# Kernel tuning notes

Measured on AMD Instinct MI355X. Metric: run time of the kernel, lower is better.

## Reference

```python
import jax, jax.numpy as jnp
import numpy as np

EMB = 1024
HEADS = 16
HEAD_DIM = EMB // HEADS


def setup_inputs() -> dict:
    key = jax.random.key(0)
    ks = jax.random.split(key, 6)
    B, T, D = 4, 2048, EMB
    s = 1.0 / np.sqrt(D)
    return {
        "x": jax.random.normal(ks[0], (B, T, D), dtype=jnp.float32),
        "Wq": jax.random.normal(ks[1], (D, D), dtype=jnp.float32) * s,
        "Wk": jax.random.normal(ks[2], (D, D), dtype=jnp.float32) * s,
        "Wv": jax.random.normal(ks[3], (D, D), dtype=jnp.float32) * s,
        "Wo": jax.random.normal(ks[4], (D, D), dtype=jnp.float32) * s,
        "bo": jax.random.normal(ks[5], (D,), dtype=jnp.float32) * 0.01,
    }


def reference(x, Wq, Wk, Wv, Wo, bo):
    B, T, D = x.shape
    H, Hd = HEADS, HEAD_DIM
    # torch Linear: x @ W.T ; here W stored [out,in]
    def heads(W):
        return (x @ W.T).reshape(B, T, H, Hd).transpose(0, 2, 1, 3)  # [B,H,T,Hd]
    Q, K, V = heads(Wq), heads(Wk), heads(Wv)
    scores = jnp.einsum("bhqd,bhkd->bhqk", Q, K) / np.sqrt(Hd)
    causal = jnp.triu(jnp.ones((T, T), dtype=bool), k=1)
    scores = jnp.where(causal, -jnp.inf, scores)
    weights = jax.nn.softmax(scores, axis=-1)  # dropout rate 0 -> identity
    ctx = jnp.einsum("bhqk,bhkd->bhqd", weights, V)
    ctx = ctx.transpose(0, 2, 1, 3).reshape(B, T, D)
    return ctx @ Wo.T + bo
```

## Files before the change

### kernel.cpp

```cpp
#include <hip/hip_runtime.h>

typedef short bf16x8 __attribute__((ext_vector_type(8)));
typedef float f32x4 __attribute__((ext_vector_type(4)));
typedef unsigned short u16;
typedef unsigned int u32;

__device__ __forceinline__ u16 f2b(float x) {
  union { float f; u32 u; } c; c.f = x;
  u32 r = (c.u + 0x7FFFu + ((c.u >> 16) & 1u)) >> 16;
  return (u16)r;
}

__device__ __forceinline__ float fexp2(float x) {
  return __builtin_amdgcn_exp2f(x);
}

__device__ __forceinline__ void glds16(const void* g, void* l) {
  __builtin_amdgcn_global_load_lds(
      (const __attribute__((address_space(1))) u32*)g,
      (__attribute__((address_space(3))) u32*)l, 16, 0, 0);
}

__global__ void cvt_all(const float* __restrict__ x, const float* __restrict__ Wq,
                        const float* __restrict__ Wk, const float* __restrict__ Wv,
                        const float* __restrict__ Wo, u16* __restrict__ xb,
                        u16* __restrict__ wqkvb, u16* __restrict__ wob, float qscale) {
  const int i = blockIdx.x * blockDim.x + threadIdx.x;
  const float* src;
  u16* dst;
  float scale = 1.0f;
  int off;
  if (i < 2097152) {
    src = x; dst = xb; off = i;
  } else {
    const int j = i - 2097152;
    const int wsel = j >> 18;
    off = j & 262143;
    if (wsel == 0)      { src = Wq; dst = wqkvb;            scale = qscale; }
    else if (wsel == 1) { src = Wk; dst = wqkvb + 1048576; }
    else if (wsel == 2) { src = Wv; dst = wqkvb + 2097152; }
    else                { src = Wo; dst = wob; }
  }
  float4 v = reinterpret_cast<const float4*>(src)[off];
  ushort4 o;
  o.x = f2b(v.x * scale); o.y = f2b(v.y * scale);
  o.z = f2b(v.z * scale); o.w = f2b(v.w * scale);
  reinterpret_cast<ushort4*>(dst)[off] = o;
}

template<int MODE>
__global__ __launch_bounds__(512, 2)
void gemm2(const u16* __restrict__ A, const u16* __restrict__ Bm,
           u16* __restrict__ Cq, u16* __restrict__ Ck, u16* __restrict__ Cvt,
           float* __restrict__ Cf, const float* __restrict__ bias) {
  constexpr int K = 1024, NKT = K / 64;
  __shared__ __attribute__((aligned(16))) u16 lds[3][24576];
  const int tid = threadIdx.x;
  const int w = tid >> 6;
  const int l = tid & 63;
  const int wm = w >> 2, wn = w & 3;
  const int lr = l & 15, lg = l >> 4;
  const int brow = blockIdx.x * 128;
  const int bcol = blockIdx.y * 256;
  const int wg = w * 64;

  const u16* Ab = A + (size_t)brow * K;
  const u16* Bb = Bm + (size_t)bcol * K;
  int gA[2], lA[2], gB[4], lB[4];
#pragma unroll
  for (int i = 0; i < 2; ++i) {
    const int q = i * 512 + tid;
    const int r = q >> 3, s = (q & 7) ^ (r & 7);
    gA[i] = r * K + s * 8;
    lA[i] = (i * 512 + wg) * 8;
  }
#pragma unroll
  for (int i = 0; i < 4; ++i) {
    const int q = i * 512 + tid;
    const int r = q >> 3, s = (q & 7) ^ (r & 7);
    gB[i] = r * K + s * 8;
    lB[i] = 8192 + (i * 512 + wg) * 8;
  }

  int aoff[4][2], boff[4][2];
#pragma unroll
  for (int m = 0; m < 4; ++m) {
    const int row = wm * 64 + m * 16 + lr;
#pragma unroll
    for (int kk = 0; kk < 2; ++kk)
      aoff[m][kk] = row * 64 + (((kk * 4 + lg) ^ (row & 7)) * 8);
  }
#pragma unroll
  for (int n = 0; n < 4; ++n) {
    const int row = wn * 64 + n * 16 + lr;
#pragma unroll
    for (int kk = 0; kk < 2; ++kk)
      boff[n][kk] = 8192 + row * 64 + (((kk * 4 + lg) ^ (row & 7)) * 8);
  }

  f32x4 acc[4][4] = {};

#pragma unroll
  for (int i = 0; i < 2; ++i) glds16(Ab + gA[i], &lds[0][lA[i]]);
#pragma unroll
  for (int i = 0; i < 4; ++i) glds16(Bb + gB[i], &lds[0][lB[i]]);
#pragma unroll
  for (int i = 0; i < 2; ++i) glds16(Ab + gA[i] + 64, &lds[1][lA[i]]);
#pragma unroll
  for (int i = 0; i < 4; ++i) glds16(Bb + gB[i] + 64, &lds[1][lB[i]]);
  asm volatile("s_waitcnt vmcnt(6)" ::: "memory");
  asm volatile("s_barrier" ::: "memory");

  int bi = 0;
  for (int kt = 0; kt < NKT; ++kt) {
    const u16* Lb = lds[bi];
    const int bs = (bi + 2 >= 3) ? (bi - 1) : (bi + 2);
    const bool st = (kt + 2 < NKT);
    const int ko = (kt + 2) * 64;

    bf16x8 a[4][2], b01[2][2];
#pragma unroll
    for (int m = 0; m < 4; ++m)
#pragma unroll
      for (int kk = 0; kk < 2; ++kk)
        a[m][kk] = *reinterpret_cast<const bf16x8*>(&Lb[aoff[m][kk]]);
#pragma unroll
    for (int n = 0; n < 2; ++n)
#pragma unroll
      for (int kk = 0; kk < 2; ++kk)
        b01[n][kk] = *reinterpret_cast<const bf16x8*>(&Lb[boff[n][kk]]);
    if (st) {
      glds16(Ab + gA[0] + ko, &lds[bs][lA[0]]);
      glds16(Ab + gA[1] + ko, &lds[bs][lA[1]]);
      glds16(Bb + gB[0] + ko, &lds[bs][lB[0]]);
    }
    asm volatile("s_barrier" ::: "memory");
    asm volatile("s_waitcnt lgkmcnt(0)" ::: "memory");
    __builtin_amdgcn_sched_barrier(0);
    __builtin_amdgcn_s_setprio(1);
#pragma unroll
    for (int m = 0; m < 4; ++m)
#pragma unroll
      for (int n = 0; n < 2; ++n)
#pragma unroll
        for (int kk = 0; kk < 2; ++kk)
          acc[m][n] = __builtin_amdgcn_mfma_f32_16x16x32_bf16(a[m][kk], b01[n][kk], acc[m][n], 0, 0, 0);
    __builtin_amdgcn_s_setprio(0);
    asm volatile("s_barrier" ::: "memory");

    bf16x8 b23[2][2];
#pragma unroll
    for (int n = 0; n < 2; ++n)
#pragma unroll
      for (int kk = 0; kk < 2; ++kk)
        b23[n][kk] = *reinterpret_cast<const bf16x8*>(&Lb[boff[n + 2][kk]]);
    if (st) {
      glds16(Bb + gB[1] + ko, &lds[bs][lB[1]]);
      glds16(Bb + gB[2] + ko, &lds[bs][lB[2]]);
      glds16(Bb + gB[3] + ko, &lds[bs][lB[3]]);
    }
    if (kt + 1 < NKT) {
      if (st) asm volatile("s_waitcnt vmcnt(6)" ::: "memory");
      else    asm volatile("s_waitcnt vmcnt(0)" ::: "memory");
    }
    asm volatile("s_barrier" ::: "memory");
    asm volatile("s_waitcnt lgkmcnt(0)" ::: "memory");
    __builtin_amdgcn_sched_barrier(0);
    __builtin_amdgcn_s_setprio(1);
#pragma unroll
    for (int m = 0; m < 4; ++m)
#pragma unroll
      for (int n = 0; n < 2; ++n)
#pragma unroll
        for (int kk = 0; kk < 2; ++kk)
          acc[m][n + 2] = __builtin_amdgcn_mfma_f32_16x16x32_bf16(a[m][kk], b23[n][kk], acc[m][n + 2], 0, 0, 0);
    __builtin_amdgcn_s_setprio(0);
    asm volatile("s_barrier" ::: "memory");

    bi = (bi + 1 >= 3) ? 0 : bi + 1;
  }

  if (MODE == 0) {
    const int seg = blockIdx.y >> 2;
    const int cbase = (blockIdx.y & 3) * 256;
    if (seg < 2) {
      u16* dst = (seg == 0) ? Cq : Ck;
#pragma unroll
      for (int m = 0; m < 4; ++m) {
        const size_t r = (size_t)(brow + wm * 64 + m * 16 + lg * 4);
#pragma unroll
        for (int n = 0; n < 4; ++n) {
          const int c = cbase + wn * 64 + n * 16 + lr;
#pragma unroll
          for (int j = 0; j < 4; ++j)
            dst[(r + j) * 1024 + c] = f2b(acc[m][n][j]);
        }
      }
    } else {
#pragma unroll
      for (int n = 0; n < 4; ++n) {
        const int c = cbase + wn * 64 + n * 16 + lr;
        const int hh = c >> 6, dd = c & 63;
#pragma unroll
        for (int m = 0; m < 4; ++m) {
          const int r0 = brow + wm * 64 + m * 16 + lg * 4;
#pragma unroll
          for (int j = 0; j < 4; ++j) {
            const int r = r0 + j;
            const int bt = r >> 11, tt = r & 2047;
            Cvt[((size_t)((bt * 16 + hh) * 64 + dd)) * 2048 + tt] = f2b(acc[m][n][j]);
          }
        }
      }
    }
  } else {
#pragma unroll
    for (int m = 0; m < 4; ++m) {
      const size_t r = (size_t)(brow + wm * 64 + m * 16 + lg * 4);
#pragma unroll
      for (int n = 0; n < 4; ++n) {
        const int c = bcol + wn * 64 + n * 16 + lr;
        const float bv = bias[c];
#pragma unroll
        for (int j = 0; j < 4; ++j)
          Cf[(r + j) * 1024 + c] = acc[m][n][j] + bv;
      }
    }
  }
}

__global__ __launch_bounds__(512, 2)
void attn_kernel(const u16* __restrict__ qb, const u16* __restrict__ kb,
                 const u16* __restrict__ vt, u16* __restrict__ ctx) {
  __shared__ __attribute__((aligned(16))) u16 Ks[2][4096];
  __shared__ __attribute__((aligned(16))) u16 Vs[2][4096];
  __shared__ __attribute__((aligned(16))) u16 Ps[8 * 2048];
  const int bid = blockIdx.x;
  const int chunk = bid >> 6;
  const int qt = (chunk < 4) ? (7 - chunk) : (chunk - 4);
  const int bh = bid & 63;
  const int bb = bh >> 4, h = bh & 15;
  const int tid = threadIdx.x, w = tid >> 6, l = tid & 63;
  const int lr = l & 15, lg = l >> 4;
  const int Qw = qt * 256 + w * 32;
  const int kvr = tid >> 3;
  const int gv = tid & 7;
  const int kvc = gv * 8;
  const int pgW = ((gv ^ (kvr & 7)) * 8);

  int prd[2];
#pragma unroll
  for (int kc = 0; kc < 2; ++kc) prd[kc] = ((kc * 4 + lg) ^ (lr & 7)) * 8;

  bf16x8 qf[2][2];
#pragma unroll
  for (int mi = 0; mi < 2; ++mi)
#pragma unroll
    for (int kc = 0; kc < 2; ++kc)
      qf[mi][kc] = *reinterpret_cast<const bf16x8*>(
          &qb[(size_t)(bb * 2048 + Qw + mi * 16 + lr) * 1024 + h * 64 + kc * 32 + lg * 8]);

  f32x4 oacc[2][4] = {};
  float lsum[2][4] = {};

  const int ntiles = 4 * qt + 4;

  bf16x8 kr, vr;
  kr = *reinterpret_cast<const bf16x8*>(&kb[(size_t)(bb * 2048 + kvr) * 1024 + h * 64 + kvc]);
  vr = *reinterpret_cast<const bf16x8*>(&vt[(size_t)(bh * 64 + kvr) * 2048 + kvc]);
  *reinterpret_cast<bf16x8*>(&Ks[0][kvr * 64 + pgW]) = kr;
  *reinterpret_cast<bf16x8*>(&Vs[0][kvr * 64 + pgW]) = vr;
  __syncthreads();
  kr = *reinterpret_cast<const bf16x8*>(&kb[(size_t)(bb * 2048 + 64 + kvr) * 1024 + h * 64 + kvc]);
  vr = *reinterpret_cast<const bf16x8*>(&vt[(size_t)(bh * 64 + kvr) * 2048 + 64 + kvc]);

  for (int t = 0; t < ntiles; ++t) {
    const int c0 = t * 64;
    const int cur = t & 1;

    if (c0 < Qw + 32) {
      const bool diag = (c0 + 63 > Qw);

      f32x4 sacc[2][4] = {};
      __builtin_amdgcn_s_setprio(1);
#pragma unroll
      for (int kc = 0; kc < 2; ++kc)
#pragma unroll
        for (int nj = 0; nj < 4; ++nj) {
          bf16x8 kf = *reinterpret_cast<const bf16x8*>(
              &Ks[cur][(nj * 16 + lr) * 64 + prd[kc]]);
#pragma unroll
          for (int mi = 0; mi < 2; ++mi)
            sacc[mi][nj] = __builtin_amdgcn_mfma_f32_16x16x32_bf16(qf[mi][kc], kf, sacc[mi][nj], 0, 0, 0);
        }
      __builtin_amdgcn_s_setprio(0);

#pragma unroll
      for (int mi = 0; mi < 2; ++mi) {
        if (diag) {
#pragma unroll
          for (int nj = 0; nj < 4; ++nj) {
            const int col = c0 + nj * 16 + lr;
#pragma unroll
            for (int j = 0; j < 4; ++j) {
              const int row = Qw + mi * 16 + lg * 4 + j;
              if (col > row) sacc[mi][nj][j] = -1e30f;
            }
          }
        }
#pragma unroll
        for (int nj = 0; nj < 4; ++nj) {
          const int cchunk = nj * 2 + (lr >> 3);
          const int coff = lr & 7;
#pragma unroll
          for (int j = 0; j < 4; ++j) {
            const float p = fexp2(sacc[mi][nj][j]);
            lsum[mi][j] += p;
            const int rowP = mi * 16 + lg * 4 + j;
            Ps[w * 2048 + rowP * 64 + ((cchunk ^ (rowP & 7)) * 8) + coff] = f2b(p);
          }
        }
      }

      __builtin_amdgcn_s_setprio(1);
#pragma unroll
      for (int kc = 0; kc < 2; ++kc) {
        bf16x8 pf[2];
#pragma unroll
        for (int mi = 0; mi < 2; ++mi) {
          const int rowP = mi * 16 + lr;
          const int cj = kc * 4 + lg;
          pf[mi] = *reinterpret_cast<const bf16x8*>(
              &Ps[w * 2048 + rowP * 64 + ((cj ^ (rowP & 7)) * 8)]);
        }
#pragma unroll
        for (int nd = 0; nd < 4; ++nd) {
          bf16x8 vf = *reinterpret_cast<const bf16x8*>(
              &Vs[cur][(nd * 16 + lr) * 64 + prd[kc]]);
#pragma unroll
          for (int mi = 0; mi < 2; ++mi)
            oacc[mi][nd] = __builtin_amdgcn_mfma_f32_16x16x32_bf16(pf[mi], vf, oacc[mi][nd], 0, 0, 0);
        }
      }
      __builtin_amdgcn_s_setprio(0);
    }

    if (t + 1 < ntiles) {
      *reinterpret_cast<bf16x8*>(&Ks[cur ^ 1][kvr * 64 + pgW]) = kr;
      *reinterpret_cast<bf16x8*>(&Vs[cur ^ 1][kvr * 64 + pgW]) = vr;
    }
    __syncthreads();
    if (t + 2 < ntiles) {
      const int c0n = c0 + 128;
      kr = *reinterpret_cast<const bf16x8*>(
          &kb[(size_t)(bb * 2048 + c0n + kvr) * 1024 + h * 64 + kvc]);
      vr = *reinterpret_cast<const bf16x8*>(
          &vt[(size_t)(bh * 64 + kvr) * 2048 + c0n + kvc]);
    }
  }

#pragma unroll
  for (int mi = 0; mi < 2; ++mi) {
#pragma unroll
    for (int x = 1; x < 16; x <<= 1)
#pragma unroll
      for (int j = 0; j < 4; ++j) lsum[mi][j] += __shfl_xor(lsum[mi][j], x, 64);
#pragma unroll
    for (int j = 0; j < 4; ++j) {
      const float inv = 1.0f / lsum[mi][j];
      const size_t r = (size_t)(bb * 2048 + Qw + mi * 16 + lg * 4 + j);
#pragma unroll
      for (int nd = 0; nd < 4; ++nd)
        ctx[r * 1024 + h * 64 + nd * 16 + lr] = f2b(oacc[mi][nd][j] * inv);
    }
  }
}

extern "C" void kernel_launch(void* const* d_in, const int* in_sizes, int n_in,
                              void* d_out, int out_size, void* d_ws, size_t ws_size,
                              hipStream_t stream) {
  const float* x = (const float*)d_in[0];
  const float* Wq = (const float*)d_in[1];
  const float* Wk = (const float*)d_in[2];
  const float* Wv = (const float*)d_in[3];
  const float* Wo = (const float*)d_in[4];
  const float* bo = (const float*)d_in[5];
  float* out = (float*)d_out;

  char* ws = (char*)d_ws;
  u16* xb = (u16*)(ws);
  u16* qb = (u16*)(ws + (16u << 20));
  u16* kb = (u16*)(ws + (32u << 20));
  u16* vtb = (u16*)(ws + (64u << 20));
  u16* wqkvb = (u16*)(ws + (80u << 20));
  u16* wob = (u16*)(ws + (88u << 20));

  const float qscale = 0.125f * 1.4426950408889634f;
  cvt_all<<<12288, 256, 0, stream>>>(x, Wq, Wk, Wv, Wo, xb, wqkvb, wob, qscale);

  gemm2<0><<<dim3(64, 12), 512, 0, stream>>>(xb, wqkvb, qb, kb, vtb, nullptr, nullptr);
  attn_kernel<<<512, 512, 0, stream>>>(qb, kb, vtb, xb);
  gemm2<1><<<dim3(64, 4), 512, 0, stream>>>(xb, wob, nullptr, nullptr, nullptr, out, bo);
}
```

Measured before the change: 172.5 us.

## Add 128x384-tile QKV GEMM and halve attention block size to 4 waves

Adds a new QKV projection kernel that uses 128x384 output tiles with K-step 32 and a double-buffered global-to-LDS load. This cuts the grid to 512 blocks (one wave on the device) instead of 768. The attention kernel moves from 512-thread blocks covering 256 query rows to 256-thread blocks covering 128 rows with occupancy 3. Blocks are scheduled heaviest-first by query tile, which should improve load balance for the causal workload. The output projection is split into its own kernel and is unchanged. Risks include the smaller K-step raising barrier overhead in the GEMM and smaller attention blocks reloading K/V tiles more often.

```diff
diff --git a/kernel.cpp b/kernel.cpp
--- a/kernel.cpp
+++ b/kernel.cpp
@@ -48,11 +48,109 @@
   reinterpret_cast<ushort4*>(dst)[off] = o;
 }
 
-template<int MODE>
 __global__ __launch_bounds__(512, 2)
-void gemm2(const u16* __restrict__ A, const u16* __restrict__ Bm,
-           u16* __restrict__ Cq, u16* __restrict__ Ck, u16* __restrict__ Cvt,
-           float* __restrict__ Cf, const float* __restrict__ bias) {
+void gemm4(const u16* __restrict__ A, const u16* __restrict__ Bm,
+           u16* __restrict__ Cq, u16* __restrict__ Ck, u16* __restrict__ Cvt) {
+  constexpr int K = 1024, NKT = 32;
+  __shared__ __attribute__((aligned(16))) u16 lds[2][16384];
+  const int tid = threadIdx.x;
+  const int w = tid >> 6, l = tid & 63;
+  const int wm = w >> 2, wn = w & 3;
+  const int lr = l & 15, lg = l >> 4;
+  const int brow = blockIdx.x * 128;
+  const int bcol = blockIdx.y * 384;
+  const u16* Ab = A + (size_t)brow * K;
+  const u16* Bb = Bm + (size_t)bcol * K;
+
+  int gA, gBo[3];
+  {
+    const int r = tid >> 2, p = tid & 3;
+    gA = r * K + ((p ^ ((r >> 1) & 3)) * 8);
+  }
+#pragma unroll
+  for (int j = 0; j < 3; ++j) {
+    const int gb = j * 512 + tid;
+    const int r = gb >> 2, p = gb & 3;
+    gBo[j] = r * K + ((p ^ ((r >> 1) & 3)) * 8);
+  }
+
+  int a_off[4], b_off[6];
+#pragma unroll
+  for (int m = 0; m < 4; ++m) {
+    const int row = wm * 64 + m * 16 + lr;
+    a_off[m] = row * 32 + ((lg ^ ((row >> 1) & 3)) * 8);
+  }
+#pragma unroll
+  for (int n = 0; n < 6; ++n) {
+    const int row = wn * 96 + n * 16 + lr;
+    b_off[n] = 4096 + row * 32 + ((lg ^ ((row >> 1) & 3)) * 8);
+  }
+
+  f32x4 acc[4][6] = {};
+
+  glds16(Ab + gA, &lds[0][w * 512]);
+#pragma unroll
+  for (int j = 0; j < 3; ++j) glds16(Bb + gBo[j], &lds[0][4096 + j * 4096 + w * 512]);
+  asm volatile("s_waitcnt vmcnt(0)" ::: "memory");
+  asm volatile("s_barrier" ::: "memory");
+
+  for (int kt = 0; kt < NKT; ++kt) {
+    const int cur = kt & 1;
+    const u16* Lb = lds[cur];
+    u16* Sb = lds[cur ^ 1];
+    if (kt + 1 < NKT) {
+      const int ko = (kt + 1) * 32;
+      glds16(Ab + gA + ko, &Sb[w * 512]);
+#pragma unroll
+      for (int j = 0; j < 3; ++j) glds16(Bb + gBo[j] + ko, &Sb[4096 + j * 4096 + w * 512]);
+    }
+    bf16x8 a[4], b[6];
+#pragma unroll
+    for (int m = 0; m < 4; ++m) a[m] = *reinterpret_cast<const bf16x8*>(&Lb[a_off[m]]);
+#pragma unroll
+    for (int n = 0; n < 6; ++n) b[n] = *reinterpret_cast<const bf16x8*>(&Lb[b_off[n]]);
+    __builtin_amdgcn_s_setprio(1);
+#pragma unroll
+    for (int m = 0; m < 4; ++m)
+#pragma unroll
+      for (int n = 0; n < 6; ++n)
+        acc[m][n] = __builtin_amdgcn_mfma_f32_16x16x32_bf16(a[m], b[n], acc[m][n], 0, 0, 0);
+    __builtin_amdgcn_s_setprio(0);
+    asm volatile("s_waitcnt vmcnt(0)" ::: "memory");
+    asm volatile("s_barrier" ::: "memory");
+  }
+
+#pragma unroll
+  for (int n = 0; n < 6; ++n) {
+    const int c = bcol + wn * 96 + n * 16 + lr;
+    const int seg = c >> 10, cs = c & 1023;
+    if (seg < 2) {
+      u16* dst = (seg == 0) ? Cq : Ck;
+#pragma unroll
+      for (int m = 0; m < 4; ++m) {
+        const int r0 = brow + wm * 64 + m * 16 + lg * 4;
+#pragma unroll
+        for (int j = 0; j < 4; ++j)
+          dst[(size_t)(r0 + j) * 1024 + cs] = f2b(acc[m][n][j]);
+      }
+    } else {
+      const int hh = cs >> 6, dd = cs & 63;
+#pragma unroll
+      for (int m = 0; m < 4; ++m) {
+        const int r0 = brow + wm * 64 + m * 16 + lg * 4;
+#pragma unroll
+        for (int j = 0; j < 4; ++j) {
+          const int r = r0 + j, bt = r >> 11, tt = r & 2047;
+          Cvt[((size_t)((bt * 16 + hh) * 64 + dd)) * 2048 + tt] = f2b(acc[m][n][j]);
+        }
+      }
+    }
+  }
+}
+
+__global__ __launch_bounds__(512, 2)
+void gemm2o(const u16* __restrict__ A, const u16* __restrict__ Bm,
+            float* __restrict__ Cf, const float* __restrict__ bias) {
   constexpr int K = 1024, NKT = K / 64;
   __shared__ __attribute__((aligned(16))) u16 lds[3][24576];
   const int tid = threadIdx.x;
@@ -180,69 +278,33 @@
     bi = (bi + 1 >= 3) ? 0 : bi + 1;
   }
 
-  if (MODE == 0) {
-    const int seg = blockIdx.y >> 2;
-    const int cbase = (blockIdx.y & 3) * 256;
-    if (seg < 2) {
-      u16* dst = (seg == 0) ? Cq : Ck;
-#pragma unroll
-      for (int m = 0; m < 4; ++m) {
-        const size_t r = (size_t)(brow + wm * 64 + m * 16 + lg * 4);
-#pragma unroll
-        for (int n = 0; n < 4; ++n) {
-          const int c = cbase + wn * 64 + n * 16 + lr;
-#pragma unroll
-          for (int j = 0; j < 4; ++j)
-            dst[(r + j) * 1024 + c] = f2b(acc[m][n][j]);
-        }
-      }
-    } else {
-#pragma unroll
-      for (int n = 0; n < 4; ++n) {
-        const int c = cbase + wn * 64 + n * 16 + lr;
-        const int hh = c >> 6, dd = c & 63;
-#pragma unroll
-        for (int m = 0; m < 4; ++m) {
-          const int r0 = brow + wm * 64 + m * 16 + lg * 4;
-#pragma unroll
-          for (int j = 0; j < 4; ++j) {
-            const int r = r0 + j;
-            const int bt = r >> 11, tt = r & 2047;
-            Cvt[((size_t)((bt * 16 + hh) * 64 + dd)) * 2048 + tt] = f2b(acc[m][n][j]);
-          }
-        }
-      }
-    }
-  } else {
-#pragma unroll
-    for (int m = 0; m < 4; ++m) {
-      const size_t r = (size_t)(brow + wm * 64 + m * 16 + lg * 4);
-#pragma unroll
-      for (int n = 0; n < 4; ++n) {
-        const int c = bcol + wn * 64 + n * 16 + lr;
-        const float bv = bias[c];
-#pragma unroll
-        for (int j = 0; j < 4; ++j)
-          Cf[(r + j) * 1024 + c] = acc[m][n][j] + bv;
-      }
-    }
-  }
-}
-
-__global__ __launch_bounds__(512, 2)
+#pragma unroll
+  for (int m = 0; m < 4; ++m) {
+    const size_t r = (size_t)(brow + wm * 64 + m * 16 + lg * 4);
+#pragma unroll
+    for (int n = 0; n < 4; ++n) {
+      const int c = bcol + wn * 64 + n * 16 + lr;
+      const float bv = bias[c];
+#pragma unroll
+      for (int j = 0; j < 4; ++j)
+        Cf[(r + j) * 1024 + c] = acc[m][n][j] + bv;
+    }
+  }
+}
+
+__global__ __launch_bounds__(256, 3)
 void attn_kernel(const u16* __restrict__ qb, const u16* __restrict__ kb,
                  const u16* __restrict__ vt, u16* __restrict__ ctx) {
   __shared__ __attribute__((aligned(16))) u16 Ks[2][4096];
   __shared__ __attribute__((aligned(16))) u16 Vs[2][4096];
-  __shared__ __attribute__((aligned(16))) u16 Ps[8 * 2048];
+  __shared__ __attribute__((aligned(16))) u16 Ps[4 * 2048];
   const int bid = blockIdx.x;
-  const int chunk = bid >> 6;
-  const int qt = (chunk < 4) ? (7 - chunk) : (chunk - 4);
+  const int qt = 15 - (bid >> 6);
   const int bh = bid & 63;
   const int bb = bh >> 4, h = bh & 15;
   const int tid = threadIdx.x, w = tid >> 6, l = tid & 63;
   const int lr = l & 15, lg = l >> 4;
-  const int Qw = qt * 256 + w * 32;
+  const int Qw = qt * 128 + w * 32;
   const int kvr = tid >> 3;
   const int gv = tid & 7;
   const int kvc = gv * 8;
@@ -263,16 +325,29 @@
   f32x4 oacc[2][4] = {};
   float lsum[2][4] = {};
 
-  const int ntiles = 4 * qt + 4;
-
-  bf16x8 kr, vr;
-  kr = *reinterpret_cast<const bf16x8*>(&kb[(size_t)(bb * 2048 + kvr) * 1024 + h * 64 + kvc]);
-  vr = *reinterpret_cast<const bf16x8*>(&vt[(size_t)(bh * 64 + kvr) * 2048 + kvc]);
-  *reinterpret_cast<bf16x8*>(&Ks[0][kvr * 64 + pgW]) = kr;
-  *reinterpret_cast<bf16x8*>(&Vs[0][kvr * 64 + pgW]) = vr;
+  const int ntiles = 2 * qt + 2;
+
+  bf16x8 kr[2], vr[2];
+#pragma unroll
+  for (int it = 0; it < 2; ++it) {
+    kr[it] = *reinterpret_cast<const bf16x8*>(
+        &kb[(size_t)(bb * 2048 + it * 32 + kvr) * 1024 + h * 64 + kvc]);
+    vr[it] = *reinterpret_cast<const bf16x8*>(
+        &vt[(size_t)(bh * 64 + it * 32 + kvr) * 2048 + kvc]);
+  }
+#pragma unroll
+  for (int it = 0; it < 2; ++it) {
+    *reinterpret_cast<bf16x8*>(&Ks[0][(it * 32 + kvr) * 64 + pgW]) = kr[it];
+    *reinterpret_cast<bf16x8*>(&Vs[0][(it * 32 + kvr) * 64 + pgW]) = vr[it];
+  }
   __syncthreads();
-  kr = *reinterpret_cast<const bf16x8*>(&kb[(size_t)(bb * 2048 + 64 + kvr) * 1024 + h * 64 + kvc]);
-  vr = *reinterpret_cast<const bf16x8*>(&vt[(size_t)(bh * 64 + kvr) * 2048 + 64 + kvc]);
+#pragma unroll
+  for (int it = 0; it < 2; ++it) {
+    kr[it] = *reinterpret_cast<const bf16x8*>(
+        &kb[(size_t)(bb * 2048 + 64 + it * 32 + kvr) * 1024 + h * 64 + kvc]);
+    vr[it] = *reinterpret_cast<const bf16x8*>(
+        &vt[(size_t)(bh * 64 + it * 32 + kvr) * 2048 + 64 + kvc]);
+  }
 
   for (int t = 0; t < ntiles; ++t) {
     const int c0 = t * 64;
@@ -346,16 +421,22 @@
     }
 
     if (t + 1 < ntiles) {
-      *reinterpret_cast<bf16x8*>(&Ks[cur ^ 1][kvr * 64 + pgW]) = kr;
-      *reinterpret_cast<bf16x8*>(&Vs[cur ^ 1][kvr * 64 + pgW]) = vr;
+#pragma unroll
+      for (int it = 0; it < 2; ++it) {
+        *reinterpret_cast<bf16x8*>(&Ks[cur ^ 1][(it * 32 + kvr) * 64 + pgW]) = kr[it];
+        *reinterpret_cast<bf16x8*>(&Vs[cur ^ 1][(it * 32 + kvr) * 64 + pgW]) = vr[it];
+      }
     }
     __syncthreads();
     if (t + 2 < ntiles) {
       const int c0n = c0 + 128;
-      kr = *reinterpret_cast<const bf16x8*>(
-          &kb[(size_t)(bb * 2048 + c0n + kvr) * 1024 + h * 64 + kvc]);
-      vr = *reinterpret_cast<const bf16x8*>(
-          &vt[(size_t)(bh * 64 + kvr) * 2048 + c0n + kvc]);
+#pragma unroll
+      for (int it = 0; it < 2; ++it) {
+        kr[it] = *reinterpret_cast<const bf16x8*>(
+            &kb[(size_t)(bb * 2048 + c0n + it * 32 + kvr) * 1024 + h * 64 + kvc]);
+        vr[it] = *reinterpret_cast<const bf16x8*>(
+            &vt[(size_t)(bh * 64 + it * 32 + kvr) * 2048 + c0n + kvc]);
+      }
     }
   }
 
@@ -398,7 +479,7 @@
   const float qscale = 0.125f * 1.4426950408889634f;
   cvt_all<<<12288, 256, 0, stream>>>(x, Wq, Wk, Wv, Wo, xb, wqkvb, wob, qscale);
 
-  gemm2<0><<<dim3(64, 12), 512, 0, stream>>>(xb, wqkvb, qb, kb, vtb, nullptr, nullptr);
-  attn_kernel<<<512, 512, 0, stream>>>(qb, kb, vtb, xb);
-  gemm2<1><<<dim3(64, 4), 512, 0, stream>>>(xb, wob, nullptr, nullptr, nullptr, out, bo);
-}
+  gemm4<<<dim3(64, 8), 512, 0, stream>>>(xb, wqkvb, qb, kb, vtb);
+  attn_kernel<<<1024, 256, 0, stream>>>(qb, kb, vtb, xb);
+  gemm2o<<<dim3(64, 4), 512, 0, stream>>>(xb, wob, out, bo);
+}
```

Result: faster. 157.4 us (-8.8%).
